# Optimization experiments

Measured on AMD Instinct MI355X. Metric: run time of the kernel, lower is better.

The kernel has to match this reference:

```python
import jax, jax.numpy as jnp
import numpy as np


def _euclidean_distances(X):
    # X: [nb_features, n_coord_rows]; pairwise euclidean distances between rows.
    sq = jnp.sum(jnp.square(X), axis=1)          # [F]
    d = -2.0 * (X @ X.T)                          # [F, F]
    d = d + sq[None, :] + sq[:, None]
    d = jnp.maximum(d, 0.0)
    return jnp.sqrt(d)


def setup_inputs() -> dict:
    key = jax.random.key(0)
    k1, k2 = jax.random.split(key)
    xs = jax.random.normal(k1, (1024, 4096), dtype=jnp.float32)
    coordinates = jax.random.normal(k2, (256, 4096), dtype=jnp.float32)
    return {"xs": xs, "coordinates": coordinates, "nb_neighbors": 16}


def reference(xs, coordinates, nb_neighbors):
    # dist over feature columns: transpose so rows are features
    dist = _euclidean_distances(coordinates.T)                # [F, F]
    _, neighbor_indexes = jax.lax.top_k(-dist, nb_neighbors)  # [F, k]
    flat_idx = neighbor_indexes.reshape(-1)                   # row-major (feature, neighbor) order
    expanded_xs = xs[:, flat_idx]                             # [B, F*k]
    expanded_coordinates = coordinates[:, flat_idx]           # [N, F*k]
    expanded_xs = expanded_xs[:, None, :, None]               # [B, 1, F*k, 1]
    expanded_coordinates = expanded_coordinates[:, None, :, None]
    return (expanded_xs, expanded_coordinates)
```

## Files before the change

kernel.cpp:

```cpp
#include <hip/hip_runtime.h>

#define NPTS 4096
#define DIM  256
#define NNB  16
#define NCAND 32
#define LTOP  12
#define CHUNKS 8
#define JCH   (NPTS / CHUNKS)
#define JITERS (JCH / 128)
#define NSTR  (CHUNKS * 2)
#define NPART (NSTR * LTOP)

using bf16x8 = __attribute__((ext_vector_type(8))) short;
using f32x4  = __attribute__((ext_vector_type(4))) float;

static __device__ __forceinline__ unsigned short f2bf(float f) {
    unsigned u = __float_as_uint(f);
    u += 0x7FFFu + ((u >> 16) & 1u);
    return (unsigned short)(u >> 16);
}

static __device__ __forceinline__ unsigned long long packki(float k, int j) {
    unsigned u = __float_as_uint(k);
    u ^= ((unsigned)((int)u >> 31)) | 0x80000000u;
    return ((unsigned long long)u << 32) | (unsigned)j;
}

__global__ __launch_bounds__(256) void transpose_kernel(const float* __restrict__ C,
                                                        float* __restrict__ Ct,
                                                        unsigned short* __restrict__ CbT) {
    __shared__ float T[64][65];
    const int t  = threadIdx.x;
    const int p0 = blockIdx.x * 64;
    const int d0 = blockIdx.y * 64;
    const int r  = t >> 4;
    const int c4 = (t & 15) * 4;
    #pragma unroll
    for (int s = 0; s < 4; ++s) {
        int dl = r + s * 16;
        float4 v = *(const float4*)&C[(size_t)(d0 + dl) * NPTS + p0 + c4];
        T[dl][c4 + 0] = v.x; T[dl][c4 + 1] = v.y;
        T[dl][c4 + 2] = v.z; T[dl][c4 + 3] = v.w;
    }
    __syncthreads();
    #pragma unroll
    for (int s = 0; s < 4; ++s) {
        int pl = r + s * 16;
        float4 v;
        v.x = T[c4 + 0][pl]; v.y = T[c4 + 1][pl];
        v.z = T[c4 + 2][pl]; v.w = T[c4 + 3][pl];
        *(float4*)&Ct[(size_t)(p0 + pl) * DIM + d0 + c4] = v;
        unsigned lo = (unsigned)f2bf(v.x) | ((unsigned)f2bf(v.y) << 16);
        unsigned hi = (unsigned)f2bf(v.z) | ((unsigned)f2bf(v.w) << 16);
        *(uint2*)&CbT[(size_t)(p0 + pl) * DIM + d0 + c4] = make_uint2(lo, hi);
    }
}

__global__ __launch_bounds__(256) void sq_kernel(const float* __restrict__ C,
                                                 float* __restrict__ sq) {
    int j = blockIdx.x * 256 + threadIdx.x;
    float s = 0.0f;
    for (int d = 0; d < DIM; ++d) {
        float v = C[(size_t)d * NPTS + j];
        s = fmaf(v, v, s);
    }
    sq[j] = s;
}

__global__ __launch_bounds__(256) void gemm_select_kernel(
    const unsigned short* __restrict__ CbT, const float* __restrict__ sq,
    unsigned long long* __restrict__ parts)
{
    __shared__ float tile[128][65];
    const int t    = threadIdx.x;
    const int wave = t >> 6, lane = t & 63;
    const int wr   = wave >> 1, wc = wave & 1;
    const int i0   = blockIdx.y * 128 + wr * 64;
    const int jc0  = blockIdx.x * JCH;
    const int lm   = lane & 15;
    const int kg   = (lane >> 4) * 8;
    const int orow = (lane >> 4) * 4;

    const int srow = t >> 1;
    const int sS   = t & 1;

    float kk[LTOP]; int jj[LTOP];
    #pragma unroll
    for (int p = 0; p < LTOP; ++p) { kk[p] = __builtin_inff(); jj[p] = 0x7FFFFFFF; }

    for (int jit = 0; jit < JITERS; ++jit) {
        const int j0 = jc0 + jit * 128 + wc * 64;
        f32x4 acc[4][4] = {};
        for (int k0 = 0; k0 < DIM; k0 += 32) {
            bf16x8 a[4], b[4];
            #pragma unroll
            for (int m = 0; m < 4; ++m)
                a[m] = *(const bf16x8*)&CbT[(size_t)(i0 + m * 16 + lm) * DIM + k0 + kg];
            #pragma unroll
            for (int n = 0; n < 4; ++n)
                b[n] = *(const bf16x8*)&CbT[(size_t)(j0 + n * 16 + lm) * DIM + k0 + kg];
            #pragma unroll
            for (int m = 0; m < 4; ++m)
                #pragma unroll
                for (int n = 0; n < 4; ++n)
                    acc[m][n] = __builtin_amdgcn_mfma_f32_16x16x32_bf16(a[m], b[n], acc[m][n], 0, 0, 0);
        }
        float sj[4];
        #pragma unroll
        for (int n = 0; n < 4; ++n) sj[n] = sq[j0 + n * 16 + lm];

        #pragma unroll
        for (int h = 0; h < 2; ++h) {
            __syncthreads();
            if (wc == h) {
                #pragma unroll
                for (int m = 0; m < 4; ++m)
                    #pragma unroll
                    for (int n = 0; n < 4; ++n)
                        #pragma unroll
                        for (int r = 0; r < 4; ++r)
                            tile[wr * 64 + m * 16 + orow + r][n * 16 + lm] =
                                fmaf(-2.0f, acc[m][n][r], sj[n]);
            }
            __syncthreads();
            const int colbase = sS * 32;
            const int jcol0   = jc0 + jit * 128 + h * 64 + colbase;
            for (int c = 0; c < 32; ++c) {
                float k = tile[srow][colbase + c];
                int   j = jcol0 + c;
                if (k < kk[LTOP - 1]) {
                    bool b[LTOP];
                    #pragma unroll
                    for (int p = 0; p < LTOP; ++p) b[p] = k < kk[p];
                    #pragma unroll
                    for (int p = LTOP - 1; p >= 1; --p) {
                        kk[p] = b[p - 1] ? kk[p - 1] : (b[p] ? k : kk[p]);
                        jj[p] = b[p - 1] ? jj[p - 1] : (b[p] ? j : jj[p]);
                    }
                    kk[0] = b[0] ? k : kk[0];
                    jj[0] = b[0] ? j : jj[0];
                }
            }
        }
    }

    const int row = blockIdx.y * 128 + srow;
    unsigned long long* dst = &parts[((size_t)row * NSTR + blockIdx.x * 2 + sS) * LTOP];
    #pragma unroll
    for (int p = 0; p < LTOP; ++p) dst[p] = packki(kk[p], jj[p]);
}

__global__ __launch_bounds__(NPART) void merge_kernel(const unsigned long long* __restrict__ parts,
                                                      int* __restrict__ cands) {
    __shared__ unsigned long long e[NPART];
    const int row = blockIdx.x;
    const int t   = threadIdx.x;
    unsigned long long mine = parts[(size_t)row * NPART + t];
    e[t] = mine;
    __syncthreads();
    int rank = 0;
    for (int o = 0; o < NPART; ++o) rank += e[o] < mine;
    if (rank < NCAND) cands[row * NCAND + rank] = (int)(mine & 0xFFFFFFFFu);
}

__global__ __launch_bounds__(64) void refine_kernel(const float* __restrict__ Ct,
                                                    const int* __restrict__ cands,
                                                    int* __restrict__ fidx) {
    __shared__ float  xi[DIM];
    __shared__ double dk[NCAND];
    __shared__ int    di[NCAND];
    const int r    = blockIdx.x;
    const int lane = threadIdx.x;
    *(float4*)&xi[lane * 4] = *(const float4*)&Ct[(size_t)r * DIM + lane * 4];
    __syncthreads();
    if (lane < NCAND) {
        int j = cands[r * NCAND + lane];
        const float* xj = &Ct[(size_t)j * DIM];
        double s = 0.0;
        for (int d = 0; d < DIM; d += 4) {
            float4 v = *(const float4*)&xj[d];
            double e0 = (double)xi[d + 0] - (double)v.x; s = fma(e0, e0, s);
            double e1 = (double)xi[d + 1] - (double)v.y; s = fma(e1, e1, s);
            double e2 = (double)xi[d + 2] - (double)v.z; s = fma(e2, e2, s);
            double e3 = (double)xi[d + 3] - (double)v.w; s = fma(e3, e3, s);
        }
        dk[lane] = s; di[lane] = j;
    }
    __syncthreads();
    if (lane < NCAND) {
        double s = dk[lane]; int j = di[lane];
        int rank = 0;
        #pragma unroll
        for (int o = 0; o < NCAND; ++o) {
            double os = dk[o]; int oj = di[o];
            rank += (os < s) || (os == s && oj < j);
        }
        if (rank < NNB) fidx[r * NNB + rank] = j;
    }
}

__global__ __launch_bounds__(256) void gather_all_kernel(const float* __restrict__ xs,
                                                         const float* __restrict__ coords,
                                                         const int* __restrict__ fidx,
                                                         float* __restrict__ out) {
    __shared__ float row[NPTS];
    const int rb    = blockIdx.y;
    const int slice = blockIdx.x;
    const int t     = threadIdx.x;
    const float* srow;
    float* drow;
    if (rb < 1024) { srow = xs + (size_t)rb * NPTS;            drow = out + (size_t)rb * 65536; }
    else           { srow = coords + (size_t)(rb - 1024) * NPTS;
                     drow = out + (size_t)1024 * 65536 + (size_t)(rb - 1024) * 65536; }
    const int cbase = slice * 32768;

    int4 ids[8];
    #pragma unroll
    for (int q = 0; q < 8; ++q)
        ids[q] = *(const int4*)&fidx[cbase + (q * 256 + t) * 4];

    #pragma unroll
    for (int s = 0; s < NPTS / 1024; ++s)
        *(float4*)&row[(s * 256 + t) * 4] = *(const float4*)&srow[(s * 256 + t) * 4];
    __syncthreads();

    for (int g = 0; g < 4; ++g) {
        int4 nxt[8];
        if (g < 3) {
            #pragma unroll
            for (int q = 0; q < 8; ++q)
                nxt[q] = *(const int4*)&fidx[cbase + ((g + 1) * 2048 + q * 256 + t) * 4];
        }
        #pragma unroll
        for (int q = 0; q < 8; ++q) {
            int c4 = cbase + (g * 2048 + q * 256 + t) * 4;
            int4 id = ids[q];
            f32x4 v;
            v[0] = row[id.x]; v[1] = row[id.y]; v[2] = row[id.z]; v[3] = row[id.w];
            __builtin_nontemporal_store(v, (f32x4*)&drow[c4]);
        }
        #pragma unroll
        for (int q = 0; q < 8; ++q) ids[q] = nxt[q];
    }
}

extern "C" void kernel_launch(void* const* d_in, const int* in_sizes, int n_in,
                              void* d_out, int out_size, void* d_ws, size_t ws_size,
                              hipStream_t stream) {
    const float* xs     = (const float*)d_in[0];
    const float* coords = (const float*)d_in[1];
    float* out = (float*)d_out;

    unsigned long long* parts = (unsigned long long*)out;
    float*          Ct    = out + 1572864;
    unsigned short* CbT   = (unsigned short*)(Ct + (size_t)NPTS * DIM);
    float*          sqv   = (float*)(CbT + (size_t)NPTS * DIM);
    int*            cands = (int*)(sqv + NPTS);
    int*            fidx  = (int*)d_ws;

    transpose_kernel<<<dim3(64, 4), 256, 0, stream>>>(coords, Ct, CbT);
    sq_kernel<<<NPTS / 256, 256, 0, stream>>>(coords, sqv);
    gemm_select_kernel<<<dim3(CHUNKS, 32), 256, 0, stream>>>(CbT, sqv, parts);
    merge_kernel<<<NPTS, NPART, 0, stream>>>(parts, cands);
    refine_kernel<<<NPTS, 64, 0, stream>>>(Ct, cands, fidx);
    gather_all_kernel<<<dim3(2, 1280), 256, 0, stream>>>(xs, coords, fidx, out);
}
```

Measured before the change: 189.9 us.

## Fuse transpose with squared norms, merge with refine, and retune select chunking

The transpose and squared-norm kernels are combined into one prep kernel that computes norms from the shared tile while it transposes. The merge and refine kernels are fused, and refine now spreads each candidate's distance across 8 threads, with the 32 partial sums reduced in shared memory. The GEMM-select split goes from 8 to 16 column chunks with a per-stream top list of 10 instead of 12, which raises grid parallelism and doubles the partial list per row that merge ranks. The fusions remove two launches and an intermediate buffer, at the cost of fewer prep blocks and a quadratic rank loop over 320 entries.

```diff
diff --git a/kernel.cpp b/kernel.cpp
--- a/kernel.cpp
+++ b/kernel.cpp
@@ -4,8 +4,8 @@
 #define DIM  256
 #define NNB  16
 #define NCAND 32
-#define LTOP  12
-#define CHUNKS 8
+#define LTOP  10
+#define CHUNKS 16
 #define JCH   (NPTS / CHUNKS)
 #define JITERS (JCH / 128)
 #define NSTR  (CHUNKS * 2)
@@ -26,45 +26,50 @@
     return ((unsigned long long)u << 32) | (unsigned)j;
 }
 
-__global__ __launch_bounds__(256) void transpose_kernel(const float* __restrict__ C,
-                                                        float* __restrict__ Ct,
-                                                        unsigned short* __restrict__ CbT) {
+__global__ __launch_bounds__(256) void prep_kernel(const float* __restrict__ C,
+                                                   float* __restrict__ Ct,
+                                                   unsigned short* __restrict__ CbT,
+                                                   float* __restrict__ sq) {
     __shared__ float T[64][65];
+    __shared__ float sqp[4][64];
     const int t  = threadIdx.x;
     const int p0 = blockIdx.x * 64;
-    const int d0 = blockIdx.y * 64;
     const int r  = t >> 4;
     const int c4 = (t & 15) * 4;
-    #pragma unroll
-    for (int s = 0; s < 4; ++s) {
-        int dl = r + s * 16;
-        float4 v = *(const float4*)&C[(size_t)(d0 + dl) * NPTS + p0 + c4];
-        T[dl][c4 + 0] = v.x; T[dl][c4 + 1] = v.y;
-        T[dl][c4 + 2] = v.z; T[dl][c4 + 3] = v.w;
-    }
-    __syncthreads();
-    #pragma unroll
-    for (int s = 0; s < 4; ++s) {
-        int pl = r + s * 16;
-        float4 v;
-        v.x = T[c4 + 0][pl]; v.y = T[c4 + 1][pl];
-        v.z = T[c4 + 2][pl]; v.w = T[c4 + 3][pl];
-        *(float4*)&Ct[(size_t)(p0 + pl) * DIM + d0 + c4] = v;
-        unsigned lo = (unsigned)f2bf(v.x) | ((unsigned)f2bf(v.y) << 16);
-        unsigned hi = (unsigned)f2bf(v.z) | ((unsigned)f2bf(v.w) << 16);
-        *(uint2*)&CbT[(size_t)(p0 + pl) * DIM + d0 + c4] = make_uint2(lo, hi);
-    }
-}
-
-__global__ __launch_bounds__(256) void sq_kernel(const float* __restrict__ C,
-                                                 float* __restrict__ sq) {
-    int j = blockIdx.x * 256 + threadIdx.x;
-    float s = 0.0f;
-    for (int d = 0; d < DIM; ++d) {
-        float v = C[(size_t)d * NPTS + j];
-        s = fmaf(v, v, s);
-    }
-    sq[j] = s;
+    const int pp = t & 63;
+    const int q  = t >> 6;
+    float part = 0.0f;
+    for (int d0 = 0; d0 < DIM; d0 += 64) {
+        __syncthreads();
+        #pragma unroll
+        for (int s = 0; s < 4; ++s) {
+            int dl = r + s * 16;
+            float4 v = *(const float4*)&C[(size_t)(d0 + dl) * NPTS + p0 + c4];
+            T[dl][c4 + 0] = v.x; T[dl][c4 + 1] = v.y;
+            T[dl][c4 + 2] = v.z; T[dl][c4 + 3] = v.w;
+        }
+        __syncthreads();
+        #pragma unroll
+        for (int s = 0; s < 4; ++s) {
+            int pl = r + s * 16;
+            float4 v;
+            v.x = T[c4 + 0][pl]; v.y = T[c4 + 1][pl];
+            v.z = T[c4 + 2][pl]; v.w = T[c4 + 3][pl];
+            *(float4*)&Ct[(size_t)(p0 + pl) * DIM + d0 + c4] = v;
+            unsigned lo = (unsigned)f2bf(v.x) | ((unsigned)f2bf(v.y) << 16);
+            unsigned hi = (unsigned)f2bf(v.z) | ((unsigned)f2bf(v.w) << 16);
+            *(uint2*)&CbT[(size_t)(p0 + pl) * DIM + d0 + c4] = make_uint2(lo, hi);
+        }
+        #pragma unroll
+        for (int dd = 0; dd < 16; ++dd) {
+            float v = T[q * 16 + dd][pp];
+            part = fmaf(v, v, part);
+        }
+    }
+    sqp[q][pp] = part;
+    __syncthreads();
+    if (t < 64)
+        sq[p0 + t] = ((sqp[0][t] + sqp[1][t]) + sqp[2][t]) + sqp[3][t];
 }
 
 __global__ __launch_bounds__(256) void gemm_select_kernel(
@@ -150,52 +155,58 @@
     for (int p = 0; p < LTOP; ++p) dst[p] = packki(kk[p], jj[p]);
 }
 
-__global__ __launch_bounds__(NPART) void merge_kernel(const unsigned long long* __restrict__ parts,
-                                                      int* __restrict__ cands) {
+__global__ __launch_bounds__(NPART) void merge_refine_kernel(
+    const unsigned long long* __restrict__ parts, const float* __restrict__ Ct,
+    int* __restrict__ fidx)
+{
     __shared__ unsigned long long e[NPART];
+    __shared__ float  xi[DIM];
+    __shared__ int    cidx[NCAND];
+    __shared__ double pd[NCAND][8];
+    __shared__ double sums[NCAND];
     const int row = blockIdx.x;
     const int t   = threadIdx.x;
+
     unsigned long long mine = parts[(size_t)row * NPART + t];
     e[t] = mine;
+    if (t < 64) *(float4*)&xi[t * 4] = *(const float4*)&Ct[(size_t)row * DIM + t * 4];
     __syncthreads();
     int rank = 0;
     for (int o = 0; o < NPART; ++o) rank += e[o] < mine;
-    if (rank < NCAND) cands[row * NCAND + rank] = (int)(mine & 0xFFFFFFFFu);
-}
-
-__global__ __launch_bounds__(64) void refine_kernel(const float* __restrict__ Ct,
-                                                    const int* __restrict__ cands,
-                                                    int* __restrict__ fidx) {
-    __shared__ float  xi[DIM];
-    __shared__ double dk[NCAND];
-    __shared__ int    di[NCAND];
-    const int r    = blockIdx.x;
-    const int lane = threadIdx.x;
-    *(float4*)&xi[lane * 4] = *(const float4*)&Ct[(size_t)r * DIM + lane * 4];
-    __syncthreads();
-    if (lane < NCAND) {
-        int j = cands[r * NCAND + lane];
+    if (rank < NCAND) cidx[rank] = (int)(mine & 0xFFFFFFFFu);
+    __syncthreads();
+
+    if (t < 256) {
+        const int c = t >> 3, sl = t & 7;
+        const int j = cidx[c];
         const float* xj = &Ct[(size_t)j * DIM];
         double s = 0.0;
-        for (int d = 0; d < DIM; d += 4) {
+        for (int d = sl * 32; d < sl * 32 + 32; d += 4) {
             float4 v = *(const float4*)&xj[d];
             double e0 = (double)xi[d + 0] - (double)v.x; s = fma(e0, e0, s);
             double e1 = (double)xi[d + 1] - (double)v.y; s = fma(e1, e1, s);
             double e2 = (double)xi[d + 2] - (double)v.z; s = fma(e2, e2, s);
             double e3 = (double)xi[d + 3] - (double)v.w; s = fma(e3, e3, s);
         }
-        dk[lane] = s; di[lane] = j;
-    }
-    __syncthreads();
-    if (lane < NCAND) {
-        double s = dk[lane]; int j = di[lane];
-        int rank = 0;
+        pd[c][sl] = s;
+    }
+    __syncthreads();
+    if (t < NCAND) {
+        double s = 0.0;
+        #pragma unroll
+        for (int sl = 0; sl < 8; ++sl) s += pd[t][sl];
+        sums[t] = s;
+    }
+    __syncthreads();
+    if (t < NCAND) {
+        double s = sums[t]; int j = cidx[t];
+        int rk = 0;
         #pragma unroll
         for (int o = 0; o < NCAND; ++o) {
-            double os = dk[o]; int oj = di[o];
-            rank += (os < s) || (os == s && oj < j);
-        }
-        if (rank < NNB) fidx[r * NNB + rank] = j;
+            double os = sums[o]; int oj = cidx[o];
+            rk += (os < s) || (os == s && oj < j);
+        }
+        if (rk < NNB) fidx[row * NNB + rk] = j;
     }
 }
 
@@ -252,16 +263,13 @@
     float* out = (float*)d_out;
 
     unsigned long long* parts = (unsigned long long*)out;
-    float*          Ct    = out + 1572864;
+    float*          Ct    = out + (size_t)NPTS * NPART * 2;
     unsigned short* CbT   = (unsigned short*)(Ct + (size_t)NPTS * DIM);
     float*          sqv   = (float*)(CbT + (size_t)NPTS * DIM);
-    int*            cands = (int*)(sqv + NPTS);
     int*            fidx  = (int*)d_ws;
 
-    transpose_kernel<<<dim3(64, 4), 256, 0, stream>>>(coords, Ct, CbT);
-    sq_kernel<<<NPTS / 256, 256, 0, stream>>>(coords, sqv);
+    prep_kernel<<<64, 256, 0, stream>>>(coords, Ct, CbT, sqv);
     gemm_select_kernel<<<dim3(CHUNKS, 32), 256, 0, stream>>>(CbT, sqv, parts);
-    merge_kernel<<<NPTS, NPART, 0, stream>>>(parts, cands);
-    refine_kernel<<<NPTS, 64, 0, stream>>>(Ct, cands, fidx);
+    merge_refine_kernel<<<NPTS, NPART, 0, stream>>>(parts, Ct, fidx);
     gather_all_kernel<<<dim3(2, 1280), 256, 0, stream>>>(xs, coords, fidx, out);
 }
```

Measured after the change: 209.9 us. 1.11x slower.
